# Performance work log

Hardware: AMD Instinct MI355X
Metric: run time of the kernel (lower is better)

Reference implementation:

```python
import jax, jax.numpy as jnp
import numpy as np

N_NODES = 50000
N_EDGES = 800000
DIM = 128
BN_EPS = 1e-5


def setup_inputs() -> dict:
    key = jax.random.key(0)
    k1, k2, k3 = jax.random.split(key, 3)
    x = jax.random.normal(k1, (N_NODES, DIM), dtype=jnp.float32)
    edge_index = jax.random.randint(k2, (2, N_EDGES), 0, N_NODES, dtype=jnp.int64)
    W = jax.random.normal(k3, (DIM, DIM), dtype=jnp.float32) / np.sqrt(DIM)
    b = jnp.zeros((DIM,), dtype=jnp.float32)
    gamma = jnp.ones((DIM,), dtype=jnp.float32)
    beta = jnp.zeros((DIM,), dtype=jnp.float32)
    return {"x": x, "edge_index": edge_index, "W": W, "b": b,
            "gamma": gamma, "beta": beta}


def reference(x, edge_index, W, b, gamma, beta):
    # GCNConv(flow='target_to_source') with add_self_loops=True, edge_weight=None.
    N = x.shape[0]
    # add self loops with weight 1
    loops = jnp.tile(jnp.arange(N, dtype=edge_index.dtype)[None, :], (2, 1))
    ei = jnp.concatenate([edge_index, loops], axis=1)  # [2, E+N]
    row, col = ei[0], ei[1]
    ew = jnp.ones(ei.shape[1], dtype=x.dtype)
    # gcn_norm: for flow != 'source_to_target', degree is computed on row index
    deg = jax.ops.segment_sum(ew, row, num_segments=N)
    dinv = jnp.where(deg > 0, deg ** -0.5, 0.0)
    norm = dinv[row] * ew * dinv[col]  # [E+N]
    xw = x @ W  # [N, D] linear transform (no bias inside, bias added after agg)
    # flow='target_to_source': message from col (target), aggregate at row (source)
    msg = xw[col] * norm[:, None]      # [E+N, D] gather + scale
    out = jax.ops.segment_sum(msg, row, num_segments=N) + b  # scatter-add
    # BatchNorm1d (training-mode batch statistics)
    mean = out.mean(axis=0)
    var = out.var(axis=0)
    y = (out - mean) * jax.lax.rsqrt(var + BN_EPS) * gamma + beta
    # ReLU + residual
    return jax.nn.relu(y) + x
```

## Files before the change

kernel.cpp:

```cpp
#include <hip/hip_runtime.h>

#define DIM 128
#define BN_EPS 1e-5f
#define CAP 64

typedef __attribute__((ext_vector_type(8))) short short8;
typedef __attribute__((ext_vector_type(4))) float f32x4;

static __host__ size_t align256(size_t x) { return (x + 255) & ~(size_t)255; }

__device__ __forceinline__ unsigned short f2bf(float f) {
    unsigned int u = __float_as_uint(f);
    unsigned int r = (u + 0x7fffu + ((u >> 16) & 1u)) >> 16;
    return (unsigned short)r;
}

__global__ __launch_bounds__(256) void k_prep(const float* __restrict__ W,
                                              unsigned short* __restrict__ Wt,
                                              int* __restrict__ cursor,
                                              float* __restrict__ stats, int N) {
    int t = blockIdx.x * 256 + threadIdx.x;
    if (t < DIM * DIM) {
        int n = t >> 7, k = t & 127;
        Wt[t] = f2bf(W[k * DIM + n]);
    }
    if (t < N) cursor[t] = t << 6;
    if (t < 256) stats[t] = 0.f;
}

__global__ __launch_bounds__(256) void k_gemm_fill(const float* __restrict__ x,
                                                   const unsigned short* __restrict__ Wt,
                                                   const int* __restrict__ ei,
                                                   int* __restrict__ cursor,
                                                   int* __restrict__ bucket,
                                                   unsigned short* __restrict__ xw,
                                                   int N, int E, int Gg) {
    const int tid = threadIdx.x;
    if (blockIdx.x >= Gg) {
        const int f = blockIdx.x - Gg;
        const int part = f & 7;
        const int bi = f >> 3;
        const int nb = (gridDim.x - Gg) >> 3;
        const int psz = (N + 7) >> 3;
        const int lo = part * psz;
        const int hi = (lo + psz < N) ? lo + psz : N;
        for (int e = bi * 256 + tid; e < E; e += nb * 256) {
            int r = ei[e];
            if (r >= lo && r < hi) {
                int pos = atomicAdd(&cursor[r], 1);
                if (pos < (r << 6) + CAP) bucket[pos] = ei[E + e];
            }
        }
        return;
    }

    const int w = tid >> 6;
    const int lane = tid & 63;
    const int quad = lane >> 4;
    const int l15 = lane & 15;
    const int rbase = (blockIdx.x * 4 + w) * 32;
    if (rbase >= N) return;

    short8 a[2][4];
    #pragma unroll
    for (int s = 0; s < 2; ++s) {
        const int row = rbase + s * 16 + l15;
        #pragma unroll
        for (int kk = 0; kk < 4; ++kk) {
            short8 frag;
            if (row < N) {
                const float4* p = (const float4*)(x + (size_t)row * DIM + kk * 32 + quad * 8);
                float4 v0 = p[0], v1 = p[1];
                frag[0] = (short)f2bf(v0.x); frag[1] = (short)f2bf(v0.y);
                frag[2] = (short)f2bf(v0.z); frag[3] = (short)f2bf(v0.w);
                frag[4] = (short)f2bf(v1.x); frag[5] = (short)f2bf(v1.y);
                frag[6] = (short)f2bf(v1.z); frag[7] = (short)f2bf(v1.w);
            } else {
                frag = (short8)0;
            }
            a[s][kk] = frag;
        }
    }

    #pragma unroll
    for (int ct = 0; ct < 8; ++ct) {
        short8 bfr[4];
        #pragma unroll
        for (int kk = 0; kk < 4; ++kk)
            bfr[kk] = *(const short8*)(Wt + (ct * 16 + l15) * DIM + kk * 32 + quad * 8);
        f32x4 acc0 = {0.f, 0.f, 0.f, 0.f}, acc1 = {0.f, 0.f, 0.f, 0.f};
        #pragma unroll
        for (int kk = 0; kk < 4; ++kk) {
            acc0 = __builtin_amdgcn_mfma_f32_16x16x32_bf16(a[0][kk], bfr[kk], acc0, 0, 0, 0);
            acc1 = __builtin_amdgcn_mfma_f32_16x16x32_bf16(a[1][kk], bfr[kk], acc1, 0, 0, 0);
        }
        const int col = ct * 16 + l15;
        #pragma unroll
        for (int r = 0; r < 4; ++r) {
            int g0 = rbase + quad * 4 + r;
            if (g0 < N) xw[(size_t)g0 * DIM + col] = f2bf(acc0[r]);
            int g1 = g0 + 16;
            if (g1 < N) xw[(size_t)g1 * DIM + col] = f2bf(acc1[r]);
        }
    }
}

__global__ void k_dinv(const int* __restrict__ cursor, float* __restrict__ dinv, int N) {
    int i = blockIdx.x * blockDim.x + threadIdx.x;
    if (i < N) {
        int cnt = cursor[i] - (i << 6);
        if (cnt > CAP) cnt = CAP;
        dinv[i] = rsqrtf((float)(cnt + 1));
    }
}

__global__ __launch_bounds__(256) void k_agg(const unsigned int* __restrict__ xw_u32,
                                             const int* __restrict__ cursor,
                                             const int* __restrict__ bucket,
                                             const float* __restrict__ dinv,
                                             const float* __restrict__ b,
                                             float* __restrict__ out, int N) {
    const int node = blockIdx.x * 4 + (threadIdx.x >> 6);
    if (node >= N) return;
    const int lane = threadIdx.x & 63;
    const float di = dinv[node];
    unsigned int u = xw_u32[(size_t)node * 64 + lane];
    float ax = di * __uint_as_float(u << 16);
    float ay = di * __uint_as_float(u & 0xffff0000u);
    const int start = node << 6;
    int cnt = cursor[node] - start;
    if (cnt > CAP) cnt = CAP;
    const int epos = start + cnt;
    int e = start;
    for (; e + 7 < epos; e += 8) {
        int c[8];
        #pragma unroll
        for (int j = 0; j < 8; ++j) c[j] = bucket[e + j];
        float dc[8];
        unsigned int uu[8];
        #pragma unroll
        for (int j = 0; j < 8; ++j) {
            dc[j] = dinv[c[j]];
            uu[j] = xw_u32[(size_t)c[j] * 64 + lane];
        }
        #pragma unroll
        for (int j = 0; j < 8; ++j) {
            ax = fmaf(dc[j], __uint_as_float(uu[j] << 16), ax);
            ay = fmaf(dc[j], __uint_as_float(uu[j] & 0xffff0000u), ay);
        }
    }
    for (; e + 1 < epos; e += 2) {
        int c0 = bucket[e], c1 = bucket[e + 1];
        float d0 = dinv[c0], d1 = dinv[c1];
        unsigned int u0 = xw_u32[(size_t)c0 * 64 + lane];
        unsigned int u1 = xw_u32[(size_t)c1 * 64 + lane];
        ax = fmaf(d0, __uint_as_float(u0 << 16), ax);
        ay = fmaf(d0, __uint_as_float(u0 & 0xffff0000u), ay);
        ax = fmaf(d1, __uint_as_float(u1 << 16), ax);
        ay = fmaf(d1, __uint_as_float(u1 & 0xffff0000u), ay);
    }
    if (e < epos) {
        int c0 = bucket[e];
        float d0 = dinv[c0];
        unsigned int u0 = xw_u32[(size_t)c0 * 64 + lane];
        ax = fmaf(d0, __uint_as_float(u0 << 16), ax);
        ay = fmaf(d0, __uint_as_float(u0 & 0xffff0000u), ay);
    }
    float2 bb = ((const float2*)b)[lane];
    float2 o;
    o.x = bb.x + di * ax;
    o.y = bb.y + di * ay;
    ((float2*)out)[(size_t)node * 64 + lane] = o;
}

__global__ __launch_bounds__(256) void k_stats(const float* __restrict__ out,
                                               float* __restrict__ stats, int total) {
    __shared__ float s1[256], s2[256];
    int tid = threadIdx.x;
    float a = 0.f, sq = 0.f;
    for (int idx = blockIdx.x * 256 + tid; idx < total; idx += gridDim.x * 256) {
        float v = out[idx];
        a += v;
        sq += v * v;
    }
    s1[tid] = a;
    s2[tid] = sq;
    __syncthreads();
    if (tid < 128) {
        a = s1[tid] + s1[tid + 128];
        sq = s2[tid] + s2[tid + 128];
        atomicAdd(&stats[tid], a);
        atomicAdd(&stats[128 + tid], sq);
    }
}

__global__ void k_final(const float* __restrict__ x, const float* __restrict__ stats,
                        const float* __restrict__ gamma, const float* __restrict__ beta,
                        float* __restrict__ out, int total, float invN) {
    int gid = blockIdx.x * blockDim.x + threadIdx.x;
    if (gid >= total) return;
    int d = gid & 127;
    float mean = stats[d] * invN;
    float var = stats[128 + d] * invN - mean * mean;
    float y = (out[gid] - mean) * rsqrtf(var + BN_EPS) * gamma[d] + beta[d];
    out[gid] = fmaxf(y, 0.f) + x[gid];
}

extern "C" void kernel_launch(void* const* d_in, const int* in_sizes, int n_in,
                              void* d_out, int out_size, void* d_ws, size_t ws_size,
                              hipStream_t stream) {
    const float* x     = (const float*)d_in[0];
    const int*   ei    = (const int*)d_in[1];
    const float* W     = (const float*)d_in[2];
    const float* b     = (const float*)d_in[3];
    const float* gamma = (const float*)d_in[4];
    const float* beta  = (const float*)d_in[5];
    float* out = (float*)d_out;

    const int N = in_sizes[0] / DIM;
    const int E = in_sizes[1] / 2;
    const int total = N * DIM;
    const int Gg = (((N + 127) / 128) + 7) & ~7;
    const int Gf = 2048;

    char* ws = (char*)d_ws;
    size_t off = 0;
    float* stats = (float*)(ws + off);     off = align256(off + 1024);
    unsigned short* Wt = (unsigned short*)(ws + off); off = align256(off + (size_t)DIM * DIM * 2);
    int* cursor = (int*)(ws + off);        off = align256(off + (size_t)N * 4);
    float* dinv = (float*)(ws + off);      off = align256(off + (size_t)N * 4);
    int* bucket = (int*)(ws + off);        off = align256(off + (size_t)N * CAP * 4);
    unsigned short* xw = (unsigned short*)(ws + off);

    k_prep<<<(N + 255) / 256, 256, 0, stream>>>(W, Wt, cursor, stats, N);
    k_gemm_fill<<<Gg + Gf, 256, 0, stream>>>(x, Wt, ei, cursor, bucket, xw, N, E, Gg);
    k_dinv<<<(N + 255) / 256, 256, 0, stream>>>(cursor, dinv, N);
    k_agg<<<(N + 3) / 4, 256, 0, stream>>>((const unsigned int*)xw, cursor, bucket, dinv, b, out, N);
    k_stats<<<256, 256, 0, stream>>>(out, stats, total);
    k_final<<<(total + 255) / 256, 256, 0, stream>>>(x, stats, gamma, beta, out, total, 1.0f / N);
}
```

Before: 202.1 us.

## Fuse dinv and BN statistics into aggregation; batch atomics in bucket fill

Drops the separate dinv and stats kernels. Degree normalisation is now computed inline from the cursor counts, and per-column sum and sum-of-squares are accumulated inside a grid-strided aggregation kernel, then block-reduced and atomically added. The bucket-fill loop is unrolled by four so several atomics are in flight per thread. This saves two launches and a full re-read of the output. The cost is fewer aggregation blocks with a persistent-style loop, and the inline dinv uses the uncapped count, which differs from before if degree exceeds CAP.

```diff
diff --git a/kernel.cpp b/kernel.cpp
--- a/kernel.cpp
+++ b/kernel.cpp
@@ -41,10 +41,27 @@
         const int part = f & 7;
         const int bi = f >> 3;
         const int nb = (gridDim.x - Gg) >> 3;
+        const int S = nb * 256;
         const int psz = (N + 7) >> 3;
         const int lo = part * psz;
         const int hi = (lo + psz < N) ? lo + psz : N;
-        for (int e = bi * 256 + tid; e < E; e += nb * 256) {
+        int e = bi * 256 + tid;
+        for (; e + 3 * S < E; e += 4 * S) {
+            int r[4];
+            #pragma unroll
+            for (int j = 0; j < 4; ++j) r[j] = ei[e + j * S];
+            int pos[4];
+            bool in[4];
+            #pragma unroll
+            for (int j = 0; j < 4; ++j) {
+                in[j] = (r[j] >= lo) & (r[j] < hi);
+                if (in[j]) pos[j] = atomicAdd(&cursor[r[j]], 1);
+            }
+            #pragma unroll
+            for (int j = 0; j < 4; ++j)
+                if (in[j] && pos[j] < (r[j] << 6) + CAP) bucket[pos[j]] = ei[E + e + j * S];
+        }
+        for (; e < E; e += S) {
             int r = ei[e];
             if (r >= lo && r < hi) {
                 int pos = atomicAdd(&cursor[r], 1);
@@ -105,92 +122,90 @@
     }
 }
 
-__global__ void k_dinv(const int* __restrict__ cursor, float* __restrict__ dinv, int N) {
-    int i = blockIdx.x * blockDim.x + threadIdx.x;
-    if (i < N) {
-        int cnt = cursor[i] - (i << 6);
-        if (cnt > CAP) cnt = CAP;
-        dinv[i] = rsqrtf((float)(cnt + 1));
-    }
+__device__ __forceinline__ float dinv_of(const int* cursor, int c) {
+    return rsqrtf((float)(cursor[c] - (c << 6) + 1));
 }
 
 __global__ __launch_bounds__(256) void k_agg(const unsigned int* __restrict__ xw_u32,
                                              const int* __restrict__ cursor,
                                              const int* __restrict__ bucket,
-                                             const float* __restrict__ dinv,
                                              const float* __restrict__ b,
+                                             float* __restrict__ stats,
                                              float* __restrict__ out, int N) {
-    const int node = blockIdx.x * 4 + (threadIdx.x >> 6);
-    if (node >= N) return;
+    const int wid = threadIdx.x >> 6;
     const int lane = threadIdx.x & 63;
-    const float di = dinv[node];
-    unsigned int u = xw_u32[(size_t)node * 64 + lane];
-    float ax = di * __uint_as_float(u << 16);
-    float ay = di * __uint_as_float(u & 0xffff0000u);
-    const int start = node << 6;
-    int cnt = cursor[node] - start;
-    if (cnt > CAP) cnt = CAP;
-    const int epos = start + cnt;
-    int e = start;
-    for (; e + 7 < epos; e += 8) {
-        int c[8];
-        #pragma unroll
-        for (int j = 0; j < 8; ++j) c[j] = bucket[e + j];
-        float dc[8];
-        unsigned int uu[8];
-        #pragma unroll
-        for (int j = 0; j < 8; ++j) {
-            dc[j] = dinv[c[j]];
-            uu[j] = xw_u32[(size_t)c[j] * 64 + lane];
-        }
-        #pragma unroll
-        for (int j = 0; j < 8; ++j) {
-            ax = fmaf(dc[j], __uint_as_float(uu[j] << 16), ax);
-            ay = fmaf(dc[j], __uint_as_float(uu[j] & 0xffff0000u), ay);
-        }
-    }
-    for (; e + 1 < epos; e += 2) {
-        int c0 = bucket[e], c1 = bucket[e + 1];
-        float d0 = dinv[c0], d1 = dinv[c1];
-        unsigned int u0 = xw_u32[(size_t)c0 * 64 + lane];
-        unsigned int u1 = xw_u32[(size_t)c1 * 64 + lane];
-        ax = fmaf(d0, __uint_as_float(u0 << 16), ax);
-        ay = fmaf(d0, __uint_as_float(u0 & 0xffff0000u), ay);
-        ax = fmaf(d1, __uint_as_float(u1 << 16), ax);
-        ay = fmaf(d1, __uint_as_float(u1 & 0xffff0000u), ay);
-    }
-    if (e < epos) {
-        int c0 = bucket[e];
-        float d0 = dinv[c0];
-        unsigned int u0 = xw_u32[(size_t)c0 * 64 + lane];
-        ax = fmaf(d0, __uint_as_float(u0 << 16), ax);
-        ay = fmaf(d0, __uint_as_float(u0 & 0xffff0000u), ay);
-    }
-    float2 bb = ((const float2*)b)[lane];
-    float2 o;
-    o.x = bb.x + di * ax;
-    o.y = bb.y + di * ay;
-    ((float2*)out)[(size_t)node * 64 + lane] = o;
-}
-
-__global__ __launch_bounds__(256) void k_stats(const float* __restrict__ out,
-                                               float* __restrict__ stats, int total) {
-    __shared__ float s1[256], s2[256];
-    int tid = threadIdx.x;
-    float a = 0.f, sq = 0.f;
-    for (int idx = blockIdx.x * 256 + tid; idx < total; idx += gridDim.x * 256) {
-        float v = out[idx];
-        a += v;
-        sq += v * v;
-    }
-    s1[tid] = a;
-    s2[tid] = sq;
+    const int wstride = gridDim.x * 4;
+    float s1x = 0.f, s1y = 0.f, s2x = 0.f, s2y = 0.f;
+    const float2 bb = ((const float2*)b)[lane];
+
+    for (int node = blockIdx.x * 4 + wid; node < N; node += wstride) {
+        const int start = node << 6;
+        int cnt = cursor[node] - start;
+        const float di = rsqrtf((float)(cnt + 1));
+        if (cnt > CAP) cnt = CAP;
+        unsigned int u = xw_u32[(size_t)node * 64 + lane];
+        float ax = di * __uint_as_float(u << 16);
+        float ay = di * __uint_as_float(u & 0xffff0000u);
+        const int epos = start + cnt;
+        int e = start;
+        for (; e + 7 < epos; e += 8) {
+            int c[8];
+            #pragma unroll
+            for (int j = 0; j < 8; ++j) c[j] = bucket[e + j];
+            float dc[8];
+            unsigned int uu[8];
+            #pragma unroll
+            for (int j = 0; j < 8; ++j) {
+                dc[j] = dinv_of(cursor, c[j]);
+                uu[j] = xw_u32[(size_t)c[j] * 64 + lane];
+            }
+            #pragma unroll
+            for (int j = 0; j < 8; ++j) {
+                ax = fmaf(dc[j], __uint_as_float(uu[j] << 16), ax);
+                ay = fmaf(dc[j], __uint_as_float(uu[j] & 0xffff0000u), ay);
+            }
+        }
+        for (; e + 1 < epos; e += 2) {
+            int c0 = bucket[e], c1 = bucket[e + 1];
+            float d0 = dinv_of(cursor, c0), d1 = dinv_of(cursor, c1);
+            unsigned int u0 = xw_u32[(size_t)c0 * 64 + lane];
+            unsigned int u1 = xw_u32[(size_t)c1 * 64 + lane];
+            ax = fmaf(d0, __uint_as_float(u0 << 16), ax);
+            ay = fmaf(d0, __uint_as_float(u0 & 0xffff0000u), ay);
+            ax = fmaf(d1, __uint_as_float(u1 << 16), ax);
+            ay = fmaf(d1, __uint_as_float(u1 & 0xffff0000u), ay);
+        }
+        if (e < epos) {
+            int c0 = bucket[e];
+            float d0 = dinv_of(cursor, c0);
+            unsigned int u0 = xw_u32[(size_t)c0 * 64 + lane];
+            ax = fmaf(d0, __uint_as_float(u0 << 16), ax);
+            ay = fmaf(d0, __uint_as_float(u0 & 0xffff0000u), ay);
+        }
+        float ox = bb.x + di * ax;
+        float oy = bb.y + di * ay;
+        ((float2*)out)[(size_t)node * 64 + lane] = make_float2(ox, oy);
+        s1x += ox; s2x += ox * ox;
+        s1y += oy; s2y += oy * oy;
+    }
+
+    __shared__ float4 red[256];
+    red[threadIdx.x] = make_float4(s1x, s1y, s2x, s2y);
     __syncthreads();
-    if (tid < 128) {
-        a = s1[tid] + s1[tid + 128];
-        sq = s2[tid] + s2[tid + 128];
-        atomicAdd(&stats[tid], a);
-        atomicAdd(&stats[128 + tid], sq);
+    if (threadIdx.x < 64) {
+        float4 a0 = red[threadIdx.x];
+        float4 a1 = red[64 + threadIdx.x];
+        float4 a2 = red[128 + threadIdx.x];
+        float4 a3 = red[192 + threadIdx.x];
+        float v1x = a0.x + a1.x + a2.x + a3.x;
+        float v1y = a0.y + a1.y + a2.y + a3.y;
+        float v2x = a0.z + a1.z + a2.z + a3.z;
+        float v2y = a0.w + a1.w + a2.w + a3.w;
+        int l = threadIdx.x;
+        atomicAdd(&stats[2 * l], v1x);
+        atomicAdd(&stats[2 * l + 1], v1y);
+        atomicAdd(&stats[128 + 2 * l], v2x);
+        atomicAdd(&stats[128 + 2 * l + 1], v2y);
     }
 }
 
@@ -228,14 +243,11 @@
     float* stats = (float*)(ws + off);     off = align256(off + 1024);
     unsigned short* Wt = (unsigned short*)(ws + off); off = align256(off + (size_t)DIM * DIM * 2);
     int* cursor = (int*)(ws + off);        off = align256(off + (size_t)N * 4);
-    float* dinv = (float*)(ws + off);      off = align256(off + (size_t)N * 4);
     int* bucket = (int*)(ws + off);        off = align256(off + (size_t)N * CAP * 4);
     unsigned short* xw = (unsigned short*)(ws + off);
 
     k_prep<<<(N + 255) / 256, 256, 0, stream>>>(W, Wt, cursor, stats, N);
     k_gemm_fill<<<Gg + Gf, 256, 0, stream>>>(x, Wt, ei, cursor, bucket, xw, N, E, Gg);
-    k_dinv<<<(N + 255) / 256, 256, 0, stream>>>(cursor, dinv, N);
-    k_agg<<<(N + 3) / 4, 256, 0, stream>>>((const unsigned int*)xw, cursor, bucket, dinv, b, out, N);
-    k_stats<<<256, 256, 0, stream>>>(out, stats, total);
+    k_agg<<<1024, 256, 0, stream>>>((const unsigned int*)xw, cursor, bucket, b, stats, out, N);
     k_final<<<(total + 255) / 256, 256, 0, stream>>>(x, stats, gamma, beta, out, total, 1.0f / N);
 }
```

After: 228.5 us. 13.0% more time.
